# Kernel optimization log

Hardware: AMD Instinct MI355X
Metric: run time of the kernel (lower is better)

Reference implementation:

```python
import jax, jax.numpy as jnp
import numpy as np
from functools import partial

N = 10  # n_qubits (static)


def _rx(state, w, theta, n):
    # state: [B, 2^n] complex64; RX(theta) on wire w (wire 0 = most significant)
    B = state.shape[0]
    st = state.reshape(B, 2 ** w, 2, 2 ** (n - 1 - w))
    half = jnp.asarray(theta, state.real.dtype) * 0.5
    c = jnp.cos(half).reshape(-1, 1, 1)
    s = jnp.sin(half).reshape(-1, 1, 1)
    s0, s1 = st[:, :, 0], st[:, :, 1]
    n0 = c * s0 - 1j * s * s1
    n1 = -1j * s * s0 + c * s1
    return jnp.stack([n0, n1], axis=2).reshape(B, 2 ** n)


def _cnot(state, control, target, n):
    B = state.shape[0]
    a, bb = (control, target) if control < target else (target, control)
    st = state.reshape(B, 2 ** a, 2, 2 ** (bb - a - 1), 2, 2 ** (n - 1 - bb))
    if control == a:
        # control is axis 2, target axis 4: flip target where control==1
        c1 = jnp.flip(st[:, :, 1], axis=3)
        st = jnp.stack([st[:, :, 0], c1], axis=2)
    else:
        # control is axis 4, target axis 2: flip axis-2 slice where control==1
        c1 = jnp.flip(st[:, :, :, :, 1], axis=1)
        st = jnp.stack([st[:, :, :, :, 0], c1], axis=4)
    return st.reshape(B, 2 ** n)


def _expect_z(state, n):
    B = state.shape[0]
    probs = jnp.abs(state) ** 2  # [B, 2^n]
    es = []
    for w in range(n):
        p = probs.reshape(B, 2 ** w, 2, 2 ** (n - 1 - w))
        es.append(p[:, :, 0].sum((1, 2)) - p[:, :, 1].sum((1, 2)))
    return jnp.stack(es, axis=1)  # [B, n]


def _qlayer(x, theta, n):
    # x: [B, n] encoder angles; theta: [n] trainable RX angles
    B = x.shape[0]
    state = jnp.zeros((B, 2 ** n), jnp.complex64).at[:, 0].set(1.0)
    for w in range(n):
        state = _rx(state, w, x[:, w], n)
    for w in range(n):
        state = _rx(state, w, theta[w], n)
    for w in range(n - 1):
        state = _cnot(state, w, w + 1, n)
    state = _cnot(state, n - 1, 0, n)
    return _expect_z(state, n)


def setup_inputs() -> dict:
    key = jax.random.key(0)
    k1, k2, k3, k4 = jax.random.split(key, 4)
    T, B, D, H = 64, 256, 246, N
    inputs = jax.random.normal(k1, (T, B, D), jnp.float32)
    fan_in = D + H
    W = jax.random.normal(k2, (4, N, fan_in), jnp.float32) / np.sqrt(fan_in)
    b = jax.random.normal(k3, (4, N), jnp.float32) * 0.01
    thetas = jax.random.normal(k4, (4, N), jnp.float32)
    return {"inputs": inputs, "W": W, "b": b, "thetas": thetas}


def reference(inputs, W, b, thetas):
    T, B, D = inputs.shape
    H = thetas.shape[-1]
    qlayer4 = jax.vmap(partial(_qlayer, n=N))  # over the 4 gates

    def step(carry, x_t):
        hx, cx = carry
        comb = jnp.concatenate([x_t, hx], axis=1)          # [B, D+H]
        z = jnp.einsum('bi,goi->gbo', comb, W) + b[:, None, :]  # [4, B, n]
        gates = qlayer4(z, thetas)                          # [4, B, n]
        f = jax.nn.sigmoid(gates[0])
        i = jax.nn.sigmoid(gates[1])
        g = jnp.tanh(gates[2])
        o = jax.nn.sigmoid(gates[3])
        cx = f * cx + i * g
        hx = o * jnp.tanh(cx)
        return (hx, cx), hx

    hx0 = jnp.zeros((B, H), inputs.dtype)
    cx0 = jnp.zeros((B, H), inputs.dtype)
    (hx, cx), outputs = jax.lax.scan(step, (hx0, cx0), inputs)
    return outputs, hx, cx
```

## Files before the change

kernel.cpp:

```cpp
#include <hip/hip_runtime.h>
#include <hip/hip_bf16.h>

#define D_IN   246
#define NW     10
#define NG     4
#define NOUT   40
#define FANIN  256
#define BATCH  256
#define TSTEPS 64
#define WP_ELEMS (NG * D_IN * 16)

__global__ __launch_bounds__(256) void k_wt(const float* __restrict__ W,
                                            float* __restrict__ Wp) {
    int e = blockIdx.x * 256 + threadIdx.x;
    if (e >= WP_ELEMS) return;
    int o = e & 15;
    int i = (e >> 4) % D_IN;
    int g = e / (16 * D_IN);
    float v = (o < NW) ? W[(g * NW + o) * FANIN + i] : 0.f;
    Wp[e] = v;
}

template <int CTRL>
__device__ __forceinline__ float dpp_shr_mul(float p) {
    int up = __builtin_amdgcn_update_dpp(__float_as_int(1.0f), __float_as_int(p),
                                         CTRL, 0xF, 0xF, false);
    return p * __int_as_float(up);
}

__global__ __launch_bounds__(512) void k_fused(
    const float* __restrict__ x,
    const float* __restrict__ Wp,
    const float* __restrict__ bias,
    const float* __restrict__ theta,
    const float* __restrict__ W,
    float* __restrict__ out,
    float* __restrict__ hxout,
    float* __restrict__ cxout)
{
    const int b    = blockIdx.x;
    const int tid  = threadIdx.x;
    const int lane = tid & 63;
    const int wv   = __builtin_amdgcn_readfirstlane(tid >> 6);
    const int g    = wv & 3;
    const int kh   = wv >> 2;

    __shared__ float xl[64 * D_IN];
    __shared__ float pr[NG][64][NW];
    __shared__ float zl[TSTEPS * NOUT];

    const int o16 = lane & 15;
    const int oc  = (o16 < NW) ? o16 : 0;
    float wh[NG][NW];
    if (wv == 0) {
#pragma unroll
        for (int gg = 0; gg < NG; ++gg)
#pragma unroll
            for (int j = 0; j < NW; ++j)
                wh[gg][j] = W[(gg * NW + oc) * FANIN + D_IN + j];
    }

    for (int row = wv; row < 64; row += 8) {
        const float* src = x + ((size_t)row * BATCH + b) * D_IN;
        float* dst = xl + row * D_IN;
        for (int j = lane; j < 123; j += 64) {
            float2 v = *reinterpret_cast<const float2*>(src + 2 * j);
            *reinterpret_cast<float2*>(dst + 2 * j) = v;
        }
    }
    __syncthreads();

    {
        const int khbase = kh ? 124 : 0;
        const int npairs = kh ? 61 : 62;

        float acc[NW];
#pragma unroll
        for (int o = 0; o < NW; ++o) acc[o] = 0.f;

        const float* wg = Wp + (g * D_IN + khbase) * 16;
        const float* xr = xl + lane * D_IN + khbase;

#pragma unroll 4
        for (int ii = 0; ii < npairs; ++ii) {
            float2 xv = *reinterpret_cast<const float2*>(xr + 2 * ii);
#pragma unroll
            for (int o = 0; o < NW; ++o) {
                acc[o] = fmaf(xv.x, wg[(2 * ii)     * 16 + o], acc[o]);
                acc[o] = fmaf(xv.y, wg[(2 * ii + 1) * 16 + o], acc[o]);
            }
        }

        if (kh == 1) {
#pragma unroll
            for (int o = 0; o < NW; ++o) pr[g][lane][o] = acc[o];
        }
        __syncthreads();

        if (kh == 0) {
#pragma unroll
            for (int o = 0; o < NW; ++o) {
                float v = acc[o] + pr[g][lane][o] + bias[g * NW + o] + theta[g * NW + o];
                zl[lane * NOUT + o * NG + g] = v;
            }
        }
    }
    __syncthreads();
    if (wv != 0) return;

    float hx_s[NW];
#pragma unroll
    for (int j = 0; j < NW; ++j) hx_s[j] = 0.f;
    float cx = 0.f, hv = 0.f;

    const float* zrow = zl + oc * NG;
    float4 zn = *reinterpret_cast<const float4*>(zrow);
    float* outp = out + (size_t)b * NW + oc;

    for (int t = 0; t < TSTEPS; ++t) {
        float4 zc4 = zn;
        zn = *reinterpret_cast<const float4*>(zrow + ((t + 1) & 63) * NOUT);

        float z0 = zc4.x, z1 = zc4.y, z2 = zc4.z, z3 = zc4.w;
#pragma unroll
        for (int j = 0; j < NW; ++j) {
            z0 = fmaf(hx_s[j], wh[0][j], z0);
            z1 = fmaf(hx_s[j], wh[1][j], z1);
            z2 = fmaf(hx_s[j], wh[2][j], z2);
            z3 = fmaf(hx_s[j], wh[3][j], z3);
        }

        float p0 = __cosf(z0), p1 = __cosf(z1), p2 = __cosf(z2), p3 = __cosf(z3);

        p0 = dpp_shr_mul<0x111>(p0); p1 = dpp_shr_mul<0x111>(p1);
        p2 = dpp_shr_mul<0x111>(p2); p3 = dpp_shr_mul<0x111>(p3);
        p0 = dpp_shr_mul<0x112>(p0); p1 = dpp_shr_mul<0x112>(p1);
        p2 = dpp_shr_mul<0x112>(p2); p3 = dpp_shr_mul<0x112>(p3);
        p0 = dpp_shr_mul<0x114>(p0); p1 = dpp_shr_mul<0x114>(p1);
        p2 = dpp_shr_mul<0x114>(p2); p3 = dpp_shr_mul<0x114>(p3);
        p0 = dpp_shr_mul<0x118>(p0); p1 = dpp_shr_mul<0x118>(p1);
        p2 = dpp_shr_mul<0x118>(p2); p3 = dpp_shr_mul<0x118>(p3);

        float fg  = __fdividef(1.f, 1.f + __expf(-p0));
        float ig  = __fdividef(1.f, 1.f + __expf(-p1));
        float gg2 = 2.f * __fdividef(1.f, 1.f + __expf(-2.f * p2)) - 1.f;
        float og  = __fdividef(1.f, 1.f + __expf(-p3));

        cx = fmaf(fg, cx, ig * gg2);
        float e2 = __expf(cx + cx);
        float th = 1.f - __fdividef(2.f, 1.f + e2);
        hv = og * th;

        if (lane < NW) outp[(size_t)t * (BATCH * NW)] = hv;

#pragma unroll
        for (int j = 0; j < NW; ++j)
            hx_s[j] = __int_as_float(__builtin_amdgcn_readlane(__float_as_int(hv), j));
    }

    if (lane < NW) {
        hxout[b * NW + lane] = hv;
        cxout[b * NW + lane] = cx;
    }
}

extern "C" void kernel_launch(void* const* d_in, const int* in_sizes, int n_in,
                              void* d_out, int out_size, void* d_ws, size_t ws_size,
                              hipStream_t stream) {
    const float* x     = (const float*)d_in[0];
    const float* W     = (const float*)d_in[1];
    const float* bias  = (const float*)d_in[2];
    const float* theta = (const float*)d_in[3];

    float* out   = (float*)d_out;
    float* hxout = out + (size_t)TSTEPS * BATCH * NW;
    float* cxout = hxout + (size_t)BATCH * NW;

    float* Wp = (float*)d_ws;

    k_wt<<<(WP_ELEMS + 255) / 256, 256, 0, stream>>>(W, Wp);
    k_fused<<<BATCH, 512, 0, stream>>>(x, Wp, bias, theta, W, out, hxout, cxout);
}
```

Measured before the change: 116.6 us.

## Split fused kernel into separate input GEMM and recurrent scan kernels

Moves the input projection out of the per-batch fused kernel into its own GEMM kernel, gridded over (timestep, batch quarter). Each block now reads a contiguous 64x246 slab of x instead of strided per-batch rows. The weights are repacked as interleaved pairs so each k-pair needs five float4 loads. The scan becomes a lightweight 64-thread kernel that reads precomputed z from a workspace buffer, which costs an extra global round-trip and one more launch.

```diff
diff --git a/kernel.cpp b/kernel.cpp
--- a/kernel.cpp
+++ b/kernel.cpp
@@ -8,17 +8,92 @@
 #define FANIN  256
 #define BATCH  256
 #define TSTEPS 64
-#define WP_ELEMS (NG * D_IN * 16)
+#define NPAIR  123
+#define WPK_ELEMS (NG * NPAIR * 20)
 
 __global__ __launch_bounds__(256) void k_wt(const float* __restrict__ W,
-                                            float* __restrict__ Wp) {
+                                            float* __restrict__ Wpk) {
     int e = blockIdx.x * 256 + threadIdx.x;
-    if (e >= WP_ELEMS) return;
-    int o = e & 15;
-    int i = (e >> 4) % D_IN;
-    int g = e / (16 * D_IN);
-    float v = (o < NW) ? W[(g * NW + o) * FANIN + i] : 0.f;
-    Wp[e] = v;
+    if (e >= WPK_ELEMS) return;
+    int q = e % 20;
+    int j = (e / 20) % NPAIR;
+    int g = e / (20 * NPAIR);
+    int o = q >> 1, k = q & 1;
+    Wpk[e] = W[(g * NW + o) * FANIN + (2 * j + k)];
+}
+
+__global__ __launch_bounds__(512) void k_gemm(
+    const float* __restrict__ x,
+    const float* __restrict__ Wpk,
+    const float* __restrict__ bias,
+    const float* __restrict__ theta,
+    float* __restrict__ zxT)
+{
+    const int t    = blockIdx.x;
+    const int bq   = blockIdx.y;
+    const int tid  = threadIdx.x;
+    const int lane = tid & 63;
+    const int wv   = __builtin_amdgcn_readfirstlane(tid >> 6);
+    const int g    = wv & 3;
+    const int kh   = wv >> 2;
+
+    __shared__ float xl[64 * D_IN];
+    __shared__ float pr[NG][64][NW];
+
+    const float* xsrc = x + ((size_t)t * BATCH + bq * 64) * D_IN;
+    for (int k = tid; k < 64 * NPAIR; k += 512) {
+        int row = k / NPAIR;
+        int j   = k - row * NPAIR;
+        float2 v = *reinterpret_cast<const float2*>(xsrc + row * D_IN + 2 * j);
+        *reinterpret_cast<float2*>(xl + row * D_IN + 2 * j) = v;
+    }
+    __syncthreads();
+
+    const int jstart = kh ? 62 : 0;
+    const int npairs = kh ? 61 : 62;
+
+    unsigned long long wa = (unsigned long long)(Wpk + (g * NPAIR + jstart) * 20);
+    asm("" : "+v"(wa));
+    const float* wbase = (const float*)wa;
+
+    float acc[NW];
+#pragma unroll
+    for (int o = 0; o < NW; ++o) acc[o] = 0.f;
+
+    const float* xr = xl + lane * D_IN + 2 * jstart;
+
+#pragma unroll 4
+    for (int jj = 0; jj < npairs; ++jj) {
+        float2 xv = *reinterpret_cast<const float2*>(xr + 2 * jj);
+        const float4* w4 = reinterpret_cast<const float4*>(wbase + jj * 20);
+        float4 wa0 = w4[0], wb = w4[1], wc = w4[2], wd = w4[3], we = w4[4];
+        acc[0] = fmaf(xv.x, wa0.x, fmaf(xv.y, wa0.y, acc[0]));
+        acc[1] = fmaf(xv.x, wa0.z, fmaf(xv.y, wa0.w, acc[1]));
+        acc[2] = fmaf(xv.x, wb.x,  fmaf(xv.y, wb.y,  acc[2]));
+        acc[3] = fmaf(xv.x, wb.z,  fmaf(xv.y, wb.w,  acc[3]));
+        acc[4] = fmaf(xv.x, wc.x,  fmaf(xv.y, wc.y,  acc[4]));
+        acc[5] = fmaf(xv.x, wc.z,  fmaf(xv.y, wc.w,  acc[5]));
+        acc[6] = fmaf(xv.x, wd.x,  fmaf(xv.y, wd.y,  acc[6]));
+        acc[7] = fmaf(xv.x, wd.z,  fmaf(xv.y, wd.w,  acc[7]));
+        acc[8] = fmaf(xv.x, we.x,  fmaf(xv.y, we.y,  acc[8]));
+        acc[9] = fmaf(xv.x, we.z,  fmaf(xv.y, we.w,  acc[9]));
+    }
+
+    if (kh == 1) {
+#pragma unroll
+        for (int o = 0; o < NW; ++o) pr[g][lane][o] = acc[o];
+    }
+    __syncthreads();
+
+    if (kh == 0) {
+        const int b = bq * 64 + lane;
+        float* zo = zxT + ((size_t)b * TSTEPS + t) * NOUT + g;
+#pragma unroll
+        for (int o = 0; o < NW; ++o) {
+            float v = acc[o] + pr[g][lane][o] + bias[g * NW + o] + theta[g * NW + o];
+            zo[o * NG] = v;
+        }
+    }
 }
 
 template <int CTRL>
@@ -28,85 +103,35 @@
     return p * __int_as_float(up);
 }
 
-__global__ __launch_bounds__(512) void k_fused(
-    const float* __restrict__ x,
-    const float* __restrict__ Wp,
-    const float* __restrict__ bias,
-    const float* __restrict__ theta,
+__global__ __launch_bounds__(64) void k_scan(
+    const float* __restrict__ zxT,
     const float* __restrict__ W,
     float* __restrict__ out,
     float* __restrict__ hxout,
     float* __restrict__ cxout)
 {
     const int b    = blockIdx.x;
-    const int tid  = threadIdx.x;
-    const int lane = tid & 63;
-    const int wv   = __builtin_amdgcn_readfirstlane(tid >> 6);
-    const int g    = wv & 3;
-    const int kh   = wv >> 2;
-
-    __shared__ float xl[64 * D_IN];
-    __shared__ float pr[NG][64][NW];
+    const int lane = threadIdx.x;
+    const int o16  = lane & 15;
+    const int oc   = (o16 < NW) ? o16 : 0;
+
     __shared__ float zl[TSTEPS * NOUT];
 
-    const int o16 = lane & 15;
-    const int oc  = (o16 < NW) ? o16 : 0;
+    {
+        const float4* s4 = reinterpret_cast<const float4*>(zxT + (size_t)b * TSTEPS * NOUT);
+        float4* d4 = reinterpret_cast<float4*>(zl);
+#pragma unroll
+        for (int q = 0; q < 10; ++q) d4[q * 64 + lane] = s4[q * 64 + lane];
+    }
+
     float wh[NG][NW];
-    if (wv == 0) {
-#pragma unroll
-        for (int gg = 0; gg < NG; ++gg)
-#pragma unroll
-            for (int j = 0; j < NW; ++j)
-                wh[gg][j] = W[(gg * NW + oc) * FANIN + D_IN + j];
-    }
-
-    for (int row = wv; row < 64; row += 8) {
-        const float* src = x + ((size_t)row * BATCH + b) * D_IN;
-        float* dst = xl + row * D_IN;
-        for (int j = lane; j < 123; j += 64) {
-            float2 v = *reinterpret_cast<const float2*>(src + 2 * j);
-            *reinterpret_cast<float2*>(dst + 2 * j) = v;
-        }
-    }
+#pragma unroll
+    for (int gg = 0; gg < NG; ++gg)
+#pragma unroll
+        for (int j = 0; j < NW; ++j)
+            wh[gg][j] = W[(gg * NW + oc) * FANIN + D_IN + j];
+
     __syncthreads();
-
-    {
-        const int khbase = kh ? 124 : 0;
-        const int npairs = kh ? 61 : 62;
-
-        float acc[NW];
-#pragma unroll
-        for (int o = 0; o < NW; ++o) acc[o] = 0.f;
-
-        const float* wg = Wp + (g * D_IN + khbase) * 16;
-        const float* xr = xl + lane * D_IN + khbase;
-
-#pragma unroll 4
-        for (int ii = 0; ii < npairs; ++ii) {
-            float2 xv = *reinterpret_cast<const float2*>(xr + 2 * ii);
-#pragma unroll
-            for (int o = 0; o < NW; ++o) {
-                acc[o] = fmaf(xv.x, wg[(2 * ii)     * 16 + o], acc[o]);
-                acc[o] = fmaf(xv.y, wg[(2 * ii + 1) * 16 + o], acc[o]);
-            }
-        }
-
-        if (kh == 1) {
-#pragma unroll
-            for (int o = 0; o < NW; ++o) pr[g][lane][o] = acc[o];
-        }
-        __syncthreads();
-
-        if (kh == 0) {
-#pragma unroll
-            for (int o = 0; o < NW; ++o) {
-                float v = acc[o] + pr[g][lane][o] + bias[g * NW + o] + theta[g * NW + o];
-                zl[lane * NOUT + o * NG + g] = v;
-            }
-        }
-    }
-    __syncthreads();
-    if (wv != 0) return;
 
     float hx_s[NW];
 #pragma unroll
@@ -176,8 +201,11 @@
     float* hxout = out + (size_t)TSTEPS * BATCH * NW;
     float* cxout = hxout + (size_t)BATCH * NW;
 
-    float* Wp = (float*)d_ws;
-
-    k_wt<<<(WP_ELEMS + 255) / 256, 256, 0, stream>>>(W, Wp);
-    k_fused<<<BATCH, 512, 0, stream>>>(x, Wp, bias, theta, W, out, hxout, cxout);
-}
+    float* Wpk = (float*)d_ws;
+    float* zxT = Wpk + WPK_ELEMS;
+
+    k_wt<<<(WPK_ELEMS + 255) / 256, 256, 0, stream>>>(W, Wpk);
+    dim3 g1(TSTEPS, 4);
+    k_gemm<<<g1, 512, 0, stream>>>(x, Wpk, bias, theta, zxT);
+    k_scan<<<BATCH, 64, 0, stream>>>(zxT, W, out, hxout, cxout);
+}
```

Result: slower. 122.1 us (+4.7%).
